# Optimization experiments

Measured on AMD Instinct MI355X. Metric: run time of the kernel, lower is better.

The kernel has to match this reference:

```python
import jax, jax.numpy as jnp
import numpy as np

S, B, I, H, O = 2048, 4096, 1, 8, 1  # seq_len, batch, input_size, hidden_size, output_size


def setup_inputs() -> dict:
    key = jax.random.key(0)
    ks = jax.random.split(key, 11)
    bound = 1.0 / np.sqrt(H)  # torch LSTMCell/Linear default init range

    def p(k, shape):
        return jax.random.uniform(k, shape, jnp.float32, -bound, bound)

    return {
        "x": jax.random.normal(ks[0], (S, B, I), jnp.float32),
        "w_ih_f": p(ks[1], (4 * H, I)),
        "w_hh_f": p(ks[2], (4 * H, H)),
        "b_ih_f": p(ks[3], (4 * H,)),
        "b_hh_f": p(ks[4], (4 * H,)),
        "w_ih_b": p(ks[5], (4 * H, I)),
        "w_hh_b": p(ks[6], (4 * H, H)),
        "b_ih_b": p(ks[7], (4 * H,)),
        "b_hh_b": p(ks[8], (4 * H,)),
        "w_out": p(ks[9], (O, 2 * H)),
        "b_out": p(ks[10], (O,)),
        "future": 0,
    }


def _lstm_scan(xseq, w_ih, w_hh, b_ih, b_hh):
    """Run an LSTMCell (torch gate order i,f,g,o) over [S,B,I]; returns h seq [S,B,H]."""
    Sq, Bq, _ = xseq.shape
    Hq = w_hh.shape[1]
    # hoist the input projection out of the recurrence: one big GEMM
    xg = jnp.einsum('sbi,gi->sbg', xseq, w_ih) + b_ih + b_hh  # [S,B,4H]

    def step(carry, xg_t):
        h, c = carry
        gates = xg_t + h @ w_hh.T  # [B,4H]
        i_g, f_g, g_g, o_g = jnp.split(gates, 4, axis=-1)
        i_g = jax.nn.sigmoid(i_g)
        f_g = jax.nn.sigmoid(f_g)
        g_g = jnp.tanh(g_g)
        o_g = jax.nn.sigmoid(o_g)
        c = f_g * c + i_g * g_g
        h = o_g * jnp.tanh(c)
        return (h, c), h

    h0 = jnp.zeros((Bq, Hq), xseq.dtype)
    _, hs = jax.lax.scan(step, (h0, h0), xg)
    return hs


def reference(x, w_ih_f, w_hh_f, b_ih_f, b_hh_f, w_ih_b, w_hh_b, b_ih_b, b_hh_b, w_out, b_out, future):
    Sq, Bq, _ = x.shape
    # forward direction reads x[i]
    hf = _lstm_scan(x, w_ih_f, w_hh_f, b_ih_f, b_hh_f)  # [S,B,H]
    # backward cell reads x[future - i]; with torch negative indexing this is (future - i) mod S
    idx = (future - jnp.arange(Sq)) % Sq
    hb = _lstm_scan(x[idx], w_ih_b, w_hh_b, b_ih_b, b_hh_b)  # [S,B,H]
    # outputs[i] = Linear(cat(h_f[i], h_b[i]))
    h = jnp.concatenate([hf, hb], axis=-1)  # [S,B,2H]
    out = jnp.einsum('sbh,oh->sbo', h, w_out) + b_out  # [S,B,O]
    # torch.cat(outputs, dim=1): step-major columns -> [B, S*O]
    return out.transpose(1, 0, 2).reshape(Bq, Sq * out.shape[-1])
```

## Files before the change

kernel.cpp:

```cpp
#include <hip/hip_runtime.h>

#define SLEN  2048
#define BATCH 4096

template<int CTRL>
__device__ __forceinline__ float dppf(float v) {
    return __int_as_float(
        __builtin_amdgcn_update_dpp(0, __float_as_int(v), CTRL, 0xF, 0xF, true));
}
#define DPP_XOR1 0xB1
#define DPP_XOR2 0x4E
#define DPP_XOR3 0x1B
#define DPP_XOR7 0x141

template<int Q>
__device__ __forceinline__ float2 pkfma_init(float2 x2, float2 w, float2 b) {
    float2 dst;
    if constexpr (Q == 0)
        asm("v_pk_fma_f32 %0, %1, %2, %3 op_sel:[0,0,0] op_sel_hi:[0,1,1]"
            : "=v"(dst) : "v"(x2), "v"(w), "v"(b));
    else
        asm("v_pk_fma_f32 %0, %1, %2, %3 op_sel:[1,0,0] op_sel_hi:[1,1,1]"
            : "=v"(dst) : "v"(x2), "v"(w), "v"(b));
    return dst;
}
template<int Q>
__device__ __forceinline__ void pkfma_bc(float2& acc, float2 h2, float2 w) {
    if constexpr (Q == 0)
        asm("v_pk_fma_f32 %0, %1, %2, %0 op_sel:[0,0,0] op_sel_hi:[0,1,1]"
            : "+v"(acc) : "v"(h2), "v"(w));
    else
        asm("v_pk_fma_f32 %0, %1, %2, %0 op_sel:[1,0,0] op_sel_hi:[1,1,1]"
            : "+v"(acc) : "v"(h2), "v"(w));
}

extern "C" __global__ __launch_bounds__(256, 1)
void bilstm_kernel(const float* __restrict__ x,
                   const float* __restrict__ w_ih_f, const float* __restrict__ w_hh_f,
                   const float* __restrict__ b_ih_f, const float* __restrict__ b_hh_f,
                   const float* __restrict__ w_ih_b, const float* __restrict__ w_hh_b,
                   const float* __restrict__ b_ih_b, const float* __restrict__ b_hh_b,
                   const float* __restrict__ w_out, const float* __restrict__ b_out,
                   const int* __restrict__ future_p,
                   float* __restrict__ out)
{
    const int tid  = threadIdx.x;
    const int wv   = tid >> 6;
    const int lane = tid & 63;
    const int e    = lane >> 4;
    const int r    = lane & 15;
    const int d    = r >> 3;
    const int j    = r & 7;
    const int b    = blockIdx.x * 16 + wv * 4 + e;

    const float* wih_p = d ? w_ih_b : w_ih_f;
    const float* whh_p = d ? w_hh_b : w_hh_f;
    const float* bih_p = d ? b_ih_b : b_ih_f;
    const float* bhh_p = d ? b_hh_b : b_hh_f;

    const float SI = -1.4426950408889634f;
    const float SG = -2.8853900817779268f;

    const int M[8] = {0, 1, 2, 3, 7, 6, 5, 4};
    float2 Wif[8], Wgo[8], wih_if, wih_go, b_if, b_go;
    #pragma unroll
    for (int m = 0; m < 8; ++m) {
        const int idx = j ^ M[m];
        Wif[m].x = SI * whh_p[(0 + j) * 8 + idx];
        Wif[m].y = SI * whh_p[(8 + j) * 8 + idx];
        Wgo[m].x = SG * whh_p[(16 + j) * 8 + idx];
        Wgo[m].y = SI * whh_p[(24 + j) * 8 + idx];
    }
    wih_if.x = SI * wih_p[0 + j];   wih_if.y = SI * wih_p[8 + j];
    wih_go.x = SG * wih_p[16 + j];  wih_go.y = SI * wih_p[24 + j];
    b_if.x = SI * (bih_p[0 + j]  + bhh_p[0 + j]);
    b_if.y = SI * (bih_p[8 + j]  + bhh_p[8 + j]);
    b_go.x = SG * (bih_p[16 + j] + bhh_p[16 + j]);
    b_go.y = SI * (bih_p[24 + j] + bhh_p[24 + j]);

    const float wout = w_out[d * 8 + j];
    const float bout = b_out[0];
    const int   fut  = future_p[0];

    __shared__ float o_lds[4][8][72];
    float* o_ptr = &o_lds[wv][e * 2 + d][(j == 0) ? 0 : (32 + j)];
    float* o_base = &o_lds[wv][0][0];

    float c  = 0.0f;
    float hn = 0.0f;

    const char* xb = (const char*)x;
    unsigned voff = ((unsigned)(d ? (fut & (SLEN - 1)) : 0) * BATCH + (unsigned)b) * 4u;
    const unsigned vdelta = d ? (unsigned)(-(BATCH * 4)) : (unsigned)(BATCH * 4);
    const unsigned vmask  = (unsigned)(SLEN * BATCH * 4 - 1);

    float2 xa2[4], xb2[4];
    #pragma unroll
    for (int p = 0; p < 4; ++p) {
        xa2[p].x = *(const float*)(xb + voff); voff = (voff + vdelta) & vmask;
        xa2[p].y = *(const float*)(xb + voff); voff = (voff + vdelta) & vmask;
    }

    auto STEP = [&](float2 acc_if, float2 acc_go, int slot) {
        float2 P0, P1, P2, P3;
        P0.x = hn;
        P0.y = dppf<DPP_XOR1>(hn);
        P1.x = dppf<DPP_XOR2>(hn);
        P1.y = dppf<DPP_XOR3>(hn);
        P2.x = dppf<DPP_XOR7>(P0.x);
        P2.y = dppf<DPP_XOR7>(P0.y);
        P3.x = dppf<DPP_XOR7>(P1.x);
        P3.y = dppf<DPP_XOR7>(P1.y);

        pkfma_bc<0>(acc_if, P0, Wif[0]);  pkfma_bc<1>(acc_if, P0, Wif[1]);
        pkfma_bc<0>(acc_if, P1, Wif[2]);  pkfma_bc<1>(acc_if, P1, Wif[3]);
        pkfma_bc<0>(acc_if, P2, Wif[4]);  pkfma_bc<1>(acc_if, P2, Wif[5]);
        pkfma_bc<0>(acc_if, P3, Wif[6]);  pkfma_bc<1>(acc_if, P3, Wif[7]);
        pkfma_bc<0>(acc_go, P0, Wgo[0]);  pkfma_bc<1>(acc_go, P0, Wgo[1]);
        pkfma_bc<0>(acc_go, P1, Wgo[2]);  pkfma_bc<1>(acc_go, P1, Wgo[3]);
        pkfma_bc<0>(acc_go, P2, Wgo[4]);  pkfma_bc<1>(acc_go, P2, Wgo[5]);
        pkfma_bc<0>(acc_go, P3, Wgo[6]);  pkfma_bc<1>(acc_go, P3, Wgo[7]);

        float ei = __builtin_amdgcn_exp2f(acc_if.x);
        float ef = __builtin_amdgcn_exp2f(acc_if.y);
        float eg = __builtin_amdgcn_exp2f(acc_go.x);
        float eo = __builtin_amdgcn_exp2f(acc_go.y);
        float ei1 = 1.0f + ei, ef1 = 1.0f + ef, eg1 = 1.0f + eg, eo1 = 1.0f + eo;
        float riu = __builtin_amdgcn_rcpf(ei1 * eg1);
        float ig  = (2.0f - eg1) * riu;
        float rv  = __builtin_amdgcn_rcpf(ef1 * eo1);
        float fa  = rv * eo1;
        float oa  = rv * ef1;
        c = fmaf(fa, c, ig);
        float tc = __builtin_amdgcn_exp2f(SG * c);
        float rt = __builtin_amdgcn_rcpf(1.0f + tc);
        float T  = fmaf(2.0f, rt, -1.0f);
        hn = oa * T;

        float p = hn * wout;
        p += dppf<DPP_XOR1>(p);
        p += dppf<DPP_XOR2>(p);
        p += dppf<DPP_XOR7>(p);
        o_ptr[slot] = p;
    };

    for (int T = 0; T < SLEN; T += 32) {
        #pragma unroll
        for (int blk = 0; blk < 4; ++blk) {
            #pragma unroll
            for (int p = 0; p < 4; ++p) {
                if (blk & 1) {
                    xa2[p].x = *(const float*)(xb + voff); voff = (voff + vdelta) & vmask;
                    xa2[p].y = *(const float*)(xb + voff); voff = (voff + vdelta) & vmask;
                } else {
                    xb2[p].x = *(const float*)(xb + voff); voff = (voff + vdelta) & vmask;
                    xb2[p].y = *(const float*)(xb + voff); voff = (voff + vdelta) & vmask;
                }
            }
            #pragma unroll
            for (int p = 0; p < 4; ++p) {
                float2 x2 = (blk & 1) ? xb2[p] : xa2[p];
                STEP(pkfma_init<0>(x2, wih_if, b_if),
                     pkfma_init<0>(x2, wih_go, b_go), blk * 8 + 2 * p);
                STEP(pkfma_init<1>(x2, wih_if, b_if),
                     pkfma_init<1>(x2, wih_go, b_go), blk * 8 + 2 * p + 1);
            }
        }
        __builtin_amdgcn_wave_barrier();
        {
            const int le = lane >> 4, lo = lane & 15;
            const int bb = blockIdx.x * 16 + wv * 4 + le;
            float v0 = o_base[(le * 2 + 0) * 72 + lo]      + o_base[(le * 2 + 1) * 72 + lo];
            float v1 = o_base[(le * 2 + 0) * 72 + lo + 16] + o_base[(le * 2 + 1) * 72 + lo + 16];
            out[bb * SLEN + T + lo]      = v0 + bout;
            out[bb * SLEN + T + 16 + lo] = v1 + bout;
        }
        __builtin_amdgcn_wave_barrier();
    }
}

extern "C" void kernel_launch(void* const* d_in, const int* in_sizes, int n_in,
                              void* d_out, int out_size, void* d_ws, size_t ws_size,
                              hipStream_t stream) {
    const float* xp     = (const float*)d_in[0];
    const float* wihf   = (const float*)d_in[1];
    const float* whhf   = (const float*)d_in[2];
    const float* bihf   = (const float*)d_in[3];
    const float* bhhf   = (const float*)d_in[4];
    const float* wihb   = (const float*)d_in[5];
    const float* whhb   = (const float*)d_in[6];
    const float* bihb   = (const float*)d_in[7];
    const float* bhhb   = (const float*)d_in[8];
    const float* wo     = (const float*)d_in[9];
    const float* bo     = (const float*)d_in[10];
    const int*   futp   = (const int*)d_in[11];
    float*       outp   = (float*)d_out;

    dim3 grid(BATCH / 16);
    dim3 block(256);
    hipLaunchKernelGGL(bilstm_kernel, grid, block, 0, stream,
                       xp, wihf, whhf, bihf, bhhf, wihb, whhb, bihb, bhhb,
                       wo, bo, futp, outp);
}
```

Baseline: 297.8 us.

## Interleave two independent batch recurrences per thread to hide step latency

Each thread now advances two independent LSTM chains (batch b and b+2048) in alternation, and the grid is halved to match. The dependent chain of DPP, FMA and transcendental ops in one chain can overlap with the other chain's instructions, so stalls in the serial recurrence are hidden. In exchange the grid has half as many blocks (128 on a 256-CU part), register use roughly doubles, and LDS staging doubles.

```diff
diff --git a/kernel.cpp b/kernel.cpp
--- a/kernel.cpp
+++ b/kernel.cpp
@@ -2,6 +2,7 @@
 
 #define SLEN  2048
 #define BATCH 4096
+#define HBAT  2048
 
 template<int CTRL>
 __device__ __forceinline__ float dppf(float v) {
@@ -51,7 +52,7 @@
     const int r    = lane & 15;
     const int d    = r >> 3;
     const int j    = r & 7;
-    const int b    = blockIdx.x * 16 + wv * 4 + e;
+    const int bA   = blockIdx.x * 16 + wv * 4 + e;
 
     const float* wih_p = d ? w_ih_b : w_ih_f;
     const float* whh_p = d ? w_hh_b : w_hh_f;
@@ -82,26 +83,40 @@
     const float bout = b_out[0];
     const int   fut  = future_p[0];
 
-    __shared__ float o_lds[4][8][72];
-    float* o_ptr = &o_lds[wv][e * 2 + d][(j == 0) ? 0 : (32 + j)];
-    float* o_base = &o_lds[wv][0][0];
-
-    float c  = 0.0f;
-    float hn = 0.0f;
-
-    const char* xb = (const char*)x;
-    unsigned voff = ((unsigned)(d ? (fut & (SLEN - 1)) : 0) * BATCH + (unsigned)b) * 4u;
-    const unsigned vdelta = d ? (unsigned)(-(BATCH * 4)) : (unsigned)(BATCH * 4);
-    const unsigned vmask  = (unsigned)(SLEN * BATCH * 4 - 1);
-
-    float2 xa2[4], xb2[4];
+    __shared__ float o_lds[2][4][8][72];
+    float* o_ptrA  = &o_lds[0][wv][e * 2 + d][(j == 0) ? 0 : (32 + j)];
+    float* o_ptrB  = &o_lds[1][wv][e * 2 + d][(j == 0) ? 0 : (32 + j)];
+    float* o_baseA = &o_lds[0][wv][0][0];
+    float* o_baseB = &o_lds[1][wv][0][0];
+
+    float cA = 0.0f, hnA = 0.0f;
+    float cB = 0.0f, hnB = 0.0f;
+
+    const char* xpA = (const char*)x;
+    const char* xpB = (const char*)x + HBAT * 4;
+    const unsigned vdelta  = d ? (unsigned)(-(BATCH * 4)) : (unsigned)(BATCH * 4);
+    const unsigned vd8     = vdelta * 8u;
+    const unsigned vmask   = (unsigned)(SLEN * BATCH * 4 - 1);
+    unsigned voffs[8];
+    {
+        unsigned v0 = ((unsigned)(d ? (fut & (SLEN - 1)) : 0) * BATCH + (unsigned)bA) * 4u;
+        #pragma unroll
+        for (int u = 0; u < 8; ++u) { voffs[u] = v0; v0 = (v0 + vdelta) & vmask; }
+    }
+
+    float2 xaA[4], xqA[4], xaB[4], xqB[4];
     #pragma unroll
     for (int p = 0; p < 4; ++p) {
-        xa2[p].x = *(const float*)(xb + voff); voff = (voff + vdelta) & vmask;
-        xa2[p].y = *(const float*)(xb + voff); voff = (voff + vdelta) & vmask;
-    }
-
-    auto STEP = [&](float2 acc_if, float2 acc_go, int slot) {
+        xaA[p].x = *(const float*)(xpA + voffs[2 * p]);
+        xaA[p].y = *(const float*)(xpA + voffs[2 * p + 1]);
+        xaB[p].x = *(const float*)(xpB + voffs[2 * p]);
+        xaB[p].y = *(const float*)(xpB + voffs[2 * p + 1]);
+    }
+    #pragma unroll
+    for (int u = 0; u < 8; ++u) voffs[u] = (voffs[u] + vd8) & vmask;
+
+    auto STEP = [&](float& c, float& hn, float* o_ptr,
+                    float2 acc_if, float2 acc_go, int slot) {
         float2 P0, P1, P2, P3;
         P0.x = hn;
         P0.y = dppf<DPP_XOR1>(hn);
@@ -150,30 +165,46 @@
             #pragma unroll
             for (int p = 0; p < 4; ++p) {
                 if (blk & 1) {
-                    xa2[p].x = *(const float*)(xb + voff); voff = (voff + vdelta) & vmask;
-                    xa2[p].y = *(const float*)(xb + voff); voff = (voff + vdelta) & vmask;
+                    xaA[p].x = *(const float*)(xpA + voffs[2 * p]);
+                    xaA[p].y = *(const float*)(xpA + voffs[2 * p + 1]);
+                    xaB[p].x = *(const float*)(xpB + voffs[2 * p]);
+                    xaB[p].y = *(const float*)(xpB + voffs[2 * p + 1]);
                 } else {
-                    xb2[p].x = *(const float*)(xb + voff); voff = (voff + vdelta) & vmask;
-                    xb2[p].y = *(const float*)(xb + voff); voff = (voff + vdelta) & vmask;
+                    xqA[p].x = *(const float*)(xpA + voffs[2 * p]);
+                    xqA[p].y = *(const float*)(xpA + voffs[2 * p + 1]);
+                    xqB[p].x = *(const float*)(xpB + voffs[2 * p]);
+                    xqB[p].y = *(const float*)(xpB + voffs[2 * p + 1]);
                 }
             }
             #pragma unroll
+            for (int u = 0; u < 8; ++u) voffs[u] = (voffs[u] + vd8) & vmask;
+            #pragma unroll
             for (int p = 0; p < 4; ++p) {
-                float2 x2 = (blk & 1) ? xb2[p] : xa2[p];
-                STEP(pkfma_init<0>(x2, wih_if, b_if),
-                     pkfma_init<0>(x2, wih_go, b_go), blk * 8 + 2 * p);
-                STEP(pkfma_init<1>(x2, wih_if, b_if),
-                     pkfma_init<1>(x2, wih_go, b_go), blk * 8 + 2 * p + 1);
+                float2 xA = (blk & 1) ? xqA[p] : xaA[p];
+                float2 xB = (blk & 1) ? xqB[p] : xaB[p];
+                const int s0 = blk * 8 + 2 * p;
+                STEP(cA, hnA, o_ptrA, pkfma_init<0>(xA, wih_if, b_if),
+                     pkfma_init<0>(xA, wih_go, b_go), s0);
+                STEP(cB, hnB, o_ptrB, pkfma_init<0>(xB, wih_if, b_if),
+                     pkfma_init<0>(xB, wih_go, b_go), s0);
+                STEP(cA, hnA, o_ptrA, pkfma_init<1>(xA, wih_if, b_if),
+                     pkfma_init<1>(xA, wih_go, b_go), s0 + 1);
+                STEP(cB, hnB, o_ptrB, pkfma_init<1>(xB, wih_if, b_if),
+                     pkfma_init<1>(xB, wih_go, b_go), s0 + 1);
             }
         }
         __builtin_amdgcn_wave_barrier();
         {
             const int le = lane >> 4, lo = lane & 15;
             const int bb = blockIdx.x * 16 + wv * 4 + le;
-            float v0 = o_base[(le * 2 + 0) * 72 + lo]      + o_base[(le * 2 + 1) * 72 + lo];
-            float v1 = o_base[(le * 2 + 0) * 72 + lo + 16] + o_base[(le * 2 + 1) * 72 + lo + 16];
-            out[bb * SLEN + T + lo]      = v0 + bout;
-            out[bb * SLEN + T + 16 + lo] = v1 + bout;
+            float a0 = o_baseA[(le * 2 + 0) * 72 + lo]      + o_baseA[(le * 2 + 1) * 72 + lo];
+            float a1 = o_baseA[(le * 2 + 0) * 72 + lo + 16] + o_baseA[(le * 2 + 1) * 72 + lo + 16];
+            float q0 = o_baseB[(le * 2 + 0) * 72 + lo]      + o_baseB[(le * 2 + 1) * 72 + lo];
+            float q1 = o_baseB[(le * 2 + 0) * 72 + lo + 16] + o_baseB[(le * 2 + 1) * 72 + lo + 16];
+            out[bb * SLEN + T + lo]               = a0 + bout;
+            out[bb * SLEN + T + 16 + lo]          = a1 + bout;
+            out[(bb + HBAT) * SLEN + T + lo]      = q0 + bout;
+            out[(bb + HBAT) * SLEN + T + 16 + lo] = q1 + bout;
         }
         __builtin_amdgcn_wave_barrier();
     }
@@ -196,7 +227,7 @@
     const int*   futp   = (const int*)d_in[11];
     float*       outp   = (float*)d_out;
 
-    dim3 grid(BATCH / 16);
+    dim3 grid(HBAT / 16);
     dim3 block(256);
     hipLaunchKernelGGL(bilstm_kernel, grid, block, 0, stream,
                        xp, wihf, whhf, bihf, bhhf, wihb, whhb, bihb, bhhb,
```

Result: slower. 536.4 us (+80.1%).
